# Kernel optimization log

Hardware: AMD Instinct MI355X
Metric: run time of the kernel (lower is better)

The kernel has to match this reference:

```python
import jax, jax.numpy as jnp
import numpy as np

VOL_SHAPE = (160, 192, 160)

def setup_inputs() -> dict:
    key = jax.random.key(0)
    k1, k2 = jax.random.split(key)
    vol = jax.random.normal(k1, (2, *VOL_SHAPE, 1), dtype=jnp.float32)
    trf = jax.random.normal(k2, (2, *VOL_SHAPE, 3), dtype=jnp.float32)
    return {"vol": vol, "trf": trf}

def _warp(vol, trf):
    # vol: [B, X, Y, Z, C]; trf: [B, X, Y, Z, 3] dense displacement field ('ij' indexing)
    B = vol.shape[0]
    shape = vol.shape[1:-1]
    nd = len(shape)
    # sample locations = identity grid + displacement
    grid = jnp.stack(jnp.meshgrid(*[jnp.arange(s, dtype=vol.dtype) for s in shape], indexing='ij'), axis=-1)
    loc = grid[None] + trf  # [B, X, Y, Z, 3]
    max_f = jnp.array([s - 1 for s in shape], dtype=vol.dtype)
    max_i = jnp.array([s - 1 for s in shape], dtype=jnp.int32)
    # fill_value=None -> clamp to volume border (voxelmorph interpn semantics)
    loc = jnp.clip(loc, 0.0, max_f)
    loc0f = jnp.floor(loc)
    loc0 = jnp.clip(loc0f.astype(jnp.int32), 0, max_i)        # lower corner indices
    loc1 = jnp.clip(loc0 + 1, 0, max_i)                       # upper corner indices (clipped)
    d1 = loc1.astype(vol.dtype) - loc                          # weight for lower corner
    d0 = 1.0 - d1                                              # weight for upper corner
    b = jnp.arange(B)[:, None, None, None]
    out = jnp.zeros(vol.shape, dtype=vol.dtype)
    for c in range(2 ** nd):                                   # 8 corners, fixed small loop
        bits = [(c >> d) & 1 for d in range(nd)]
        idx = [loc1[..., d] if bits[d] else loc0[..., d] for d in range(nd)]
        w = jnp.ones(loc.shape[:-1], dtype=vol.dtype)
        for d in range(nd):
            w = w * (d0[..., d] if bits[d] else d1[..., d])
        out = out + w[..., None] * vol[b, idx[0], idx[1], idx[2]]
    return out

def reference(vol, trf):
    return _warp(vol, trf)
```

## Files before the change

### kernel.cpp

```cpp
#include <hip/hip_runtime.h>


#define NXD 160
#define NYD 192
#define NZD 160
#define NVOX (NXD * NYD * NZD)
#define NBATCH 2
#define NTOT (NBATCH * NVOX)

__global__ __launch_bounds__(256)
void warp3d_kernel(const float* __restrict__ vol,
                   const float* __restrict__ trf,
                   float* __restrict__ out) {
    int i = blockIdx.x * blockDim.x + threadIdx.x;
    if (i >= NTOT) return;

    int z  = i % NZD;
    int t  = i / NZD;
    int y  = t % NYD;
    int t2 = t / NYD;
    int x  = t2 % NXD;
    int b  = t2 / NXD;

    size_t ti = 3ull * (size_t)i;
    float tx = trf[ti + 0];
    float ty = trf[ti + 1];
    float tz = trf[ti + 2];

    float lx = fminf(fmaxf((float)x + tx, 0.0f), (float)(NXD - 1));
    float ly = fminf(fmaxf((float)y + ty, 0.0f), (float)(NYD - 1));
    float lz = fminf(fmaxf((float)z + tz, 0.0f), (float)(NZD - 1));

    float fx = floorf(lx), fy = floorf(ly), fz = floorf(lz);
    int x0 = (int)fx, y0 = (int)fy, z0 = (int)fz;
    int x1 = min(x0 + 1, NXD - 1);
    int y1 = min(y0 + 1, NYD - 1);
    int z1 = min(z0 + 1, NZD - 1);

    float wx0 = (float)x1 - lx;
    float wy0 = (float)y1 - ly;
    float wz0 = (float)z1 - lz;
    float wx1 = 1.0f - wx0;
    float wy1 = 1.0f - wy0;
    float wz1 = 1.0f - wz0;

    const float* vb = vol + (size_t)b * NVOX;
    size_t ox0 = (size_t)x0 * (NYD * NZD);
    size_t ox1 = (size_t)x1 * (NYD * NZD);
    int    oy0 = y0 * NZD;
    int    oy1 = y1 * NZD;

    float v000 = vb[ox0 + oy0 + z0];
    float v001 = vb[ox0 + oy0 + z1];
    float v010 = vb[ox0 + oy1 + z0];
    float v011 = vb[ox0 + oy1 + z1];
    float v100 = vb[ox1 + oy0 + z0];
    float v101 = vb[ox1 + oy0 + z1];
    float v110 = vb[ox1 + oy1 + z0];
    float v111 = vb[ox1 + oy1 + z1];

    float r = wx0 * (wy0 * (wz0 * v000 + wz1 * v001) +
                     wy1 * (wz0 * v010 + wz1 * v011)) +
              wx1 * (wy0 * (wz0 * v100 + wz1 * v101) +
                     wy1 * (wz0 * v110 + wz1 * v111));

    out[i] = r;
}

extern "C" void kernel_launch(void* const* d_in, const int* in_sizes, int n_in,
                              void* d_out, int out_size, void* d_ws, size_t ws_size,
                              hipStream_t stream) {
    const float* vol = (const float*)d_in[0];
    const float* trf = (const float*)d_in[1];
    float* out = (float*)d_out;

    int threads = 256;
    int blocks = (NTOT + threads - 1) / threads;
    warp3d_kernel<<<blocks, threads, 0, stream>>>(vol, trf, out);
}
```

Baseline: 267.5 us.

## Process four voxels per thread with vectorized loads and paired z gathers

```diff
diff --git a/kernel.cpp b/kernel.cpp
--- a/kernel.cpp
+++ b/kernel.cpp
@@ -7,64 +7,99 @@
 #define NVOX (NXD * NYD * NZD)
 #define NBATCH 2
 #define NTOT (NBATCH * NVOX)
+#define VPT 4
+#define NTHREADS (NTOT / VPT)
+
+typedef float f2a4 __attribute__((ext_vector_type(2), aligned(4)));
+typedef float f4   __attribute__((ext_vector_type(4)));
 
 __global__ __launch_bounds__(256)
 void warp3d_kernel(const float* __restrict__ vol,
                    const float* __restrict__ trf,
                    float* __restrict__ out) {
-    int i = blockIdx.x * blockDim.x + threadIdx.x;
-    if (i >= NTOT) return;
+    int tid = blockIdx.x * 256 + threadIdx.x;
+    if (tid >= NTHREADS) return;
 
-    int z  = i % NZD;
-    int t  = i / NZD;
-    int y  = t % NYD;
-    int t2 = t / NYD;
-    int x  = t2 % NXD;
-    int b  = t2 / NXD;
+    int zq = tid % (NZD / VPT);
+    int r  = tid / (NZD / VPT);
+    int y  = r % NYD;
+    int r2 = r / NYD;
+    int x  = r2 % NXD;
+    int b  = r2 / NXD;
+    int zbase = zq * VPT;
 
-    size_t ti = 3ull * (size_t)i;
-    float tx = trf[ti + 0];
-    float ty = trf[ti + 1];
-    float tz = trf[ti + 2];
-
-    float lx = fminf(fmaxf((float)x + tx, 0.0f), (float)(NXD - 1));
-    float ly = fminf(fmaxf((float)y + ty, 0.0f), (float)(NYD - 1));
-    float lz = fminf(fmaxf((float)z + tz, 0.0f), (float)(NZD - 1));
-
-    float fx = floorf(lx), fy = floorf(ly), fz = floorf(lz);
-    int x0 = (int)fx, y0 = (int)fy, z0 = (int)fz;
-    int x1 = min(x0 + 1, NXD - 1);
-    int y1 = min(y0 + 1, NYD - 1);
-    int z1 = min(z0 + 1, NZD - 1);
-
-    float wx0 = (float)x1 - lx;
-    float wy0 = (float)y1 - ly;
-    float wz0 = (float)z1 - lz;
-    float wx1 = 1.0f - wx0;
-    float wy1 = 1.0f - wy0;
-    float wz1 = 1.0f - wz0;
+    const f4* trfv = (const f4*)(trf + (size_t)tid * 12);
+    f4 t0 = trfv[0];
+    f4 t1 = trfv[1];
+    f4 t2 = trfv[2];
+    float tx[VPT] = {t0.x, t0.w, t1.z, t2.y};
+    float ty[VPT] = {t0.y, t1.x, t1.w, t2.z};
+    float tz[VPT] = {t0.z, t1.y, t2.x, t2.w};
 
     const float* vb = vol + (size_t)b * NVOX;
-    size_t ox0 = (size_t)x0 * (NYD * NZD);
-    size_t ox1 = (size_t)x1 * (NYD * NZD);
-    int    oy0 = y0 * NZD;
-    int    oy1 = y1 * NZD;
 
-    float v000 = vb[ox0 + oy0 + z0];
-    float v001 = vb[ox0 + oy0 + z1];
-    float v010 = vb[ox0 + oy1 + z0];
-    float v011 = vb[ox0 + oy1 + z1];
-    float v100 = vb[ox1 + oy0 + z0];
-    float v101 = vb[ox1 + oy0 + z1];
-    float v110 = vb[ox1 + oy1 + z0];
-    float v111 = vb[ox1 + oy1 + z1];
+    f2a4  g00[VPT], g01[VPT], g10[VPT], g11[VPT];
+    float wx0[VPT], wy0[VPT], wz0[VPT];
+    int   selz[VPT];
 
-    float r = wx0 * (wy0 * (wz0 * v000 + wz1 * v001) +
-                     wy1 * (wz0 * v010 + wz1 * v011)) +
-              wx1 * (wy0 * (wz0 * v100 + wz1 * v101) +
-                     wy1 * (wz0 * v110 + wz1 * v111));
+#pragma unroll
+    for (int j = 0; j < VPT; ++j) {
+        float lx = fminf(fmaxf((float)x + tx[j], 0.0f), (float)(NXD - 1));
+        float ly = fminf(fmaxf((float)y + ty[j], 0.0f), (float)(NYD - 1));
+        float lz = fminf(fmaxf((float)(zbase + j) + tz[j], 0.0f), (float)(NZD - 1));
 
-    out[i] = r;
+        int x0 = (int)lx;
+        int y0 = (int)ly;
+        int z0 = (int)lz;
+        int x1 = min(x0 + 1, NXD - 1);
+        int y1 = min(y0 + 1, NYD - 1);
+        int z1 = min(z0 + 1, NZD - 1);
+
+        wx0[j] = (float)x1 - lx;
+        wy0[j] = (float)y1 - ly;
+        wz0[j] = (float)z1 - lz;
+
+        int zb = min(z0, NZD - 2);
+        selz[j] = (z0 == zb);
+
+        size_t ox0 = (size_t)x0 * (NYD * NZD);
+        size_t ox1 = (size_t)x1 * (NYD * NZD);
+        int    oy0 = y0 * NZD;
+        int    oy1 = y1 * NZD;
+
+        g00[j] = *(const f2a4*)(vb + ox0 + oy0 + zb);
+        g01[j] = *(const f2a4*)(vb + ox0 + oy1 + zb);
+        g10[j] = *(const f2a4*)(vb + ox1 + oy0 + zb);
+        g11[j] = *(const f2a4*)(vb + ox1 + oy1 + zb);
+    }
+
+    f4 res;
+#pragma unroll
+    for (int j = 0; j < VPT; ++j) {
+        float v000 = selz[j] ? g00[j].x : g00[j].y;
+        float v010 = selz[j] ? g01[j].x : g01[j].y;
+        float v100 = selz[j] ? g10[j].x : g10[j].y;
+        float v110 = selz[j] ? g11[j].x : g11[j].y;
+        float v001 = g00[j].y;
+        float v011 = g01[j].y;
+        float v101 = g10[j].y;
+        float v111 = g11[j].y;
+
+        float wx1 = 1.0f - wx0[j];
+        float wy1 = 1.0f - wy0[j];
+        float wz1 = 1.0f - wz0[j];
+
+        float rj = wx0[j] * (wy0[j] * (wz0[j] * v000 + wz1 * v001) +
+                             wy1    * (wz0[j] * v010 + wz1 * v011)) +
+                   wx1    * (wy0[j] * (wz0[j] * v100 + wz1 * v101) +
+                             wy1    * (wz0[j] * v110 + wz1 * v111));
+        if (j == 0) res.x = rj;
+        else if (j == 1) res.y = rj;
+        else if (j == 2) res.z = rj;
+        else res.w = rj;
+    }
+
+    *(f4*)(out + (size_t)tid * VPT) = res;
 }
 
 extern "C" void kernel_launch(void* const* d_in, const int* in_sizes, int n_in,
@@ -75,6 +110,6 @@
     float* out = (float*)d_out;
 
     int threads = 256;
-    int blocks = (NTOT + threads - 1) / threads;
+    int blocks = (NTHREADS + threads - 1) / threads;
     warp3d_kernel<<<blocks, threads, 0, stream>>>(vol, trf, out);
 }
```

After: 253.9 us. 5.1% less time.

## Stage halo volume tile in LDS and gather trilinear corners from shared memory

Applied to the files above, without the earlier changes.

```diff
diff --git a/kernel.cpp b/kernel.cpp
--- a/kernel.cpp
+++ b/kernel.cpp
@@ -6,65 +6,130 @@
 #define NZD 160
 #define NVOX (NXD * NYD * NZD)
 #define NBATCH 2
-#define NTOT (NBATCH * NVOX)
+
+#define TX 8
+#define TY 8
+#define TZ 16
+#define LXT 16
+#define LYT 16
+#define LZT 32
+#define LDS_N (LXT * LYT * LZT)
+
+#define TILES_X (NXD / TX)
+#define TILES_Y (NYD / TY)
+#define TILES_Z (NZD / TZ)
+#define NBLOCKS (NBATCH * TILES_X * TILES_Y * TILES_Z)
+
+typedef float f4 __attribute__((ext_vector_type(4)));
 
 __global__ __launch_bounds__(256)
 void warp3d_kernel(const float* __restrict__ vol,
                    const float* __restrict__ trf,
                    float* __restrict__ out) {
-    int i = blockIdx.x * blockDim.x + threadIdx.x;
-    if (i >= NTOT) return;
+    __shared__ float tile[LDS_N];
 
-    int z  = i % NZD;
-    int t  = i / NZD;
-    int y  = t % NYD;
-    int t2 = t / NYD;
-    int x  = t2 % NXD;
-    int b  = t2 / NXD;
+    int bid = blockIdx.x;
+    int tz = bid % TILES_Z;
+    int r  = bid / TILES_Z;
+    int ty = r % TILES_Y;
+    int r2 = r / TILES_Y;
+    int tx = r2 % TILES_X;
+    int b  = r2 / TILES_X;
 
-    size_t ti = 3ull * (size_t)i;
-    float tx = trf[ti + 0];
-    float ty = trf[ti + 1];
-    float tz = trf[ti + 2];
-
-    float lx = fminf(fmaxf((float)x + tx, 0.0f), (float)(NXD - 1));
-    float ly = fminf(fmaxf((float)y + ty, 0.0f), (float)(NYD - 1));
-    float lz = fminf(fmaxf((float)z + tz, 0.0f), (float)(NZD - 1));
-
-    float fx = floorf(lx), fy = floorf(ly), fz = floorf(lz);
-    int x0 = (int)fx, y0 = (int)fy, z0 = (int)fz;
-    int x1 = min(x0 + 1, NXD - 1);
-    int y1 = min(y0 + 1, NYD - 1);
-    int z1 = min(z0 + 1, NZD - 1);
-
-    float wx0 = (float)x1 - lx;
-    float wy0 = (float)y1 - ly;
-    float wz0 = (float)z1 - lz;
-    float wx1 = 1.0f - wx0;
-    float wy1 = 1.0f - wy0;
-    float wz1 = 1.0f - wz0;
+    int x0t = tx * TX, y0t = ty * TY, z0t = tz * TZ;
+    int lox = x0t - 4, loy = y0t - 4, loz = z0t - 8;
 
     const float* vb = vol + (size_t)b * NVOX;
-    size_t ox0 = (size_t)x0 * (NYD * NZD);
-    size_t ox1 = (size_t)x1 * (NYD * NZD);
-    int    oy0 = y0 * NZD;
-    int    oy1 = y1 * NZD;
 
-    float v000 = vb[ox0 + oy0 + z0];
-    float v001 = vb[ox0 + oy0 + z1];
-    float v010 = vb[ox0 + oy1 + z0];
-    float v011 = vb[ox0 + oy1 + z1];
-    float v100 = vb[ox1 + oy0 + z0];
-    float v101 = vb[ox1 + oy0 + z1];
-    float v110 = vb[ox1 + oy1 + z0];
-    float v111 = vb[ox1 + oy1 + z1];
+    int t = threadIdx.x;
+    int zq = t & 3, yq = (t >> 2) & 7, xq = t >> 5;
+    int x = x0t + xq, y = y0t + yq, zb0 = z0t + zq * 4;
+    size_t vox_i = (((size_t)b * NXD + x) * NYD + y) * NZD + zb0;
 
-    float r = wx0 * (wy0 * (wz0 * v000 + wz1 * v001) +
-                     wy1 * (wz0 * v010 + wz1 * v011)) +
-              wx1 * (wy0 * (wz0 * v100 + wz1 * v101) +
-                     wy1 * (wz0 * v110 + wz1 * v111));
+    const f4* trfv = (const f4*)(trf + vox_i * 3);
+    f4 t0 = trfv[0], t1 = trfv[1], t2 = trfv[2];
 
-    out[i] = r;
+    bool interior = (lox >= 0) & (lox + LXT <= NXD) &
+                    (loy >= 0) & (loy + LYT <= NYD) &
+                    (loz >= 0) & (loz + LZT <= NZD);
+    if (interior) {
+        const float* gbase = vb + ((size_t)(lox * NYD + loy) * NZD + loz);
+        int w = t >> 6;
+        int l = t & 63;
+#pragma unroll
+        for (int it = 0; it < 8; ++it) {
+            int chunk = it * 4 + w;
+            int p = chunk * 256 + l * 4;
+            int zi = p & 31, yi = (p >> 5) & 15, xi = p >> 9;
+            const float* g = gbase + (size_t)xi * (NYD * NZD) + yi * NZD + zi;
+            __builtin_amdgcn_global_load_lds(
+                (const __attribute__((address_space(1))) void*)g,
+                (__attribute__((address_space(3))) void*)&tile[chunk * 256],
+                16, 0, 0);
+        }
+    } else {
+#pragma unroll 4
+        for (int it = 0; it < LDS_N / 256; ++it) {
+            int e = it * 256 + t;
+            int zi = e & 31, yi = (e >> 5) & 15, xi = e >> 9;
+            int gx = min(max(lox + xi, 0), NXD - 1);
+            int gy = min(max(loy + yi, 0), NYD - 1);
+            int gz = min(max(loz + zi, 0), NZD - 1);
+            tile[e] = vb[(size_t)(gx * NYD + gy) * NZD + gz];
+        }
+    }
+    __syncthreads();
+
+    float dxa[4] = {t0.x, t0.w, t1.z, t2.y};
+    float dya[4] = {t0.y, t1.x, t1.w, t2.z};
+    float dza[4] = {t0.z, t1.y, t2.x, t2.w};
+
+    float res[4];
+#pragma unroll
+    for (int j = 0; j < 4; ++j) {
+        float lx = fminf(fmaxf((float)x + dxa[j], 0.0f), (float)(NXD - 1));
+        float ly = fminf(fmaxf((float)y + dya[j], 0.0f), (float)(NYD - 1));
+        float lz = fminf(fmaxf((float)(zb0 + j) + dza[j], 0.0f), (float)(NZD - 1));
+        float fx = floorf(lx), fy = floorf(ly), fz = floorf(lz);
+        int x0 = (int)fx, y0 = (int)fy, z0 = (int)fz;
+        float wx0 = fminf(fx + 1.0f, (float)(NXD - 1)) - lx;
+        float wy0 = fminf(fy + 1.0f, (float)(NYD - 1)) - ly;
+        float wz0 = fminf(fz + 1.0f, (float)(NZD - 1)) - lz;
+
+        int ix = x0 - lox, iy = y0 - loy, iz = z0 - loz;
+        bool ok = ((unsigned)ix <= LXT - 2) & ((unsigned)iy <= LYT - 2) &
+                  ((unsigned)iz <= LZT - 2);
+        int a = ok ? ((ix * LYT + iy) * LZT + iz) : 0;
+
+        float v000 = tile[a],                 v001 = tile[a + 1];
+        float v010 = tile[a + LZT],           v011 = tile[a + LZT + 1];
+        float v100 = tile[a + LYT * LZT],     v101 = tile[a + LYT * LZT + 1];
+        float v110 = tile[a + LYT * LZT + LZT], v111 = tile[a + LYT * LZT + LZT + 1];
+
+        if (!ok) {
+            int x1 = min(x0 + 1, NXD - 1);
+            int y1 = min(y0 + 1, NYD - 1);
+            int z1 = min(z0 + 1, NZD - 1);
+            size_t o00 = (size_t)(x0 * NYD + y0) * NZD;
+            size_t o01 = (size_t)(x0 * NYD + y1) * NZD;
+            size_t o10 = (size_t)(x1 * NYD + y0) * NZD;
+            size_t o11 = (size_t)(x1 * NYD + y1) * NZD;
+            v000 = vb[o00 + z0]; v001 = vb[o00 + z1];
+            v010 = vb[o01 + z0]; v011 = vb[o01 + z1];
+            v100 = vb[o10 + z0]; v101 = vb[o10 + z1];
+            v110 = vb[o11 + z0]; v111 = vb[o11 + z1];
+        }
+
+        float wx1 = 1.0f - wx0, wy1 = 1.0f - wy0, wz1 = 1.0f - wz0;
+        res[j] = wx0 * (wy0 * (wz0 * v000 + wz1 * v001) +
+                        wy1 * (wz0 * v010 + wz1 * v011)) +
+                 wx1 * (wy0 * (wz0 * v100 + wz1 * v101) +
+                        wy1 * (wz0 * v110 + wz1 * v111));
+    }
+
+    f4 o;
+    o.x = res[0]; o.y = res[1]; o.z = res[2]; o.w = res[3];
+    *(f4*)(out + vox_i) = o;
 }
 
 extern "C" void kernel_launch(void* const* d_in, const int* in_sizes, int n_in,
@@ -74,7 +139,5 @@
     const float* trf = (const float*)d_in[1];
     float* out = (float*)d_out;
 
-    int threads = 256;
-    int blocks = (NTOT + threads - 1) / threads;
-    warp3d_kernel<<<blocks, threads, 0, stream>>>(vol, trf, out);
+    warp3d_kernel<<<NBLOCKS, 256, 0, stream>>>(vol, trf, out);
 }
```

Measured after the change: 225.7 us. 15.6% less time.
